# Kernel tuning notes

Hardware: AMD Instinct MI355X
Metric: run time of the kernel (lower is better)

The kernel has to match this reference:

```python
import jax, jax.numpy as jnp
import numpy as np

N_NODES = 100000
N_EDGES = 1600000
EMB = 128
N_LAYER = 5
X_DIM = 178
E_DIM = 18
BN_EPS = 1e-5


def setup_inputs() -> dict:
    key = jax.random.key(0)
    ks = jax.random.split(key, 20)
    s = 0.05  # weight scale
    inp = {}
    inp["x"] = jax.random.normal(ks[0], (N_NODES, X_DIM), jnp.float32)
    inp["edge_attr"] = jax.random.uniform(ks[1], (N_EDGES, E_DIM), jnp.float32)
    # input MLP (178 -> emb -> emb, LeakyReLU 0.1)
    inp["iw1"] = jax.random.normal(ks[2], (X_DIM, EMB), jnp.float32) * s
    inp["ib1"] = jax.random.normal(ks[3], (EMB,), jnp.float32) * s
    inp["iw2"] = jax.random.normal(ks[4], (EMB, EMB), jnp.float32) * s
    inp["ib2"] = jax.random.normal(ks[5], (EMB,), jnp.float32) * s
    # per-layer edge embedding MLP (18 -> emb -> emb, LeakyReLU 0.1)
    inp["ew1"] = jax.random.normal(ks[6], (N_LAYER, E_DIM, EMB), jnp.float32) * s
    inp["eb1"] = jax.random.normal(ks[7], (N_LAYER, EMB), jnp.float32) * s
    inp["ew2"] = jax.random.normal(ks[8], (N_LAYER, EMB, EMB), jnp.float32) * s
    inp["eb2"] = jax.random.normal(ks[9], (N_LAYER, EMB), jnp.float32) * s
    # per-layer GIN update MLP (emb -> 2emb -> emb, ReLU)
    inp["mw1"] = jax.random.normal(ks[10], (N_LAYER, EMB, 2 * EMB), jnp.float32) * s
    inp["mb1"] = jax.random.normal(ks[11], (N_LAYER, 2 * EMB), jnp.float32) * s
    inp["mw2"] = jax.random.normal(ks[12], (N_LAYER, 2 * EMB, EMB), jnp.float32) * s
    inp["mb2"] = jax.random.normal(ks[13], (N_LAYER, EMB), jnp.float32) * s
    # per-layer BatchNorm affine params
    inp["gamma"] = jnp.ones((N_LAYER, EMB), jnp.float32)
    inp["beta"] = jnp.zeros((N_LAYER, EMB), jnp.float32)
    inp["edge_index"] = jax.random.randint(ks[14], (2, N_EDGES), 0, N_NODES)
    return inp


def _leaky(v):
    return jnp.where(v > 0, v, 0.1 * v)


def reference(x, edge_attr, iw1, ib1, iw2, ib2, ew1, eb1, ew2, eb2,
              mw1, mb1, mw2, mb2, gamma, beta, edge_index):
    src = edge_index[0]  # x_j gathered from source nodes (PyG source_to_target)
    dst = edge_index[1]
    n = x.shape[0]

    # input node MLP with LeakyReLU(0.1)
    h = _leaky(x @ iw1 + ib1) @ iw2 + ib2  # [N, EMB]

    for l in range(N_LAYER):
        # edge embeddings for real edges: [E, EMB]
        ee = _leaky(edge_attr @ ew1[l] + eb1[l]) @ ew2[l] + eb2[l]
        # self-loop edges have zero edge_attr -> constant embedding vector [EMB]
        self_e = _leaky(eb1[l]) @ ew2[l] + eb2[l]
        # message = x_j + edge_emb; aggregate (add) at destination, plus self-loop term
        msg = h[src] + ee
        aggr = jax.ops.segment_sum(msg, dst, num_segments=n) + h + self_e
        # GIN update MLP (ReLU)
        hh = jnp.maximum(aggr @ mw1[l] + mb1[l], 0.0) @ mw2[l] + mb2[l]
        # BatchNorm1d (training mode: batch stats, biased variance)
        mean = hh.mean(axis=0)
        var = hh.var(axis=0)
        hh = (hh - mean) / jnp.sqrt(var + BN_EPS) * gamma[l] + beta[l]
        if l < N_LAYER - 1:
            hh = jnp.maximum(hh, 0.0)  # ReLU on all but last layer; dropout p=0 is a no-op
        h = hh

    return h  # JK == 'last'
```

## Files before the change

kernel.cpp:

```cpp
#include <hip/hip_runtime.h>
#include <hip/hip_bf16.h>
#include <hip/hip_fp16.h>
#include <cstdint>
#include <cstddef>

#define NNODES 100000
#define NEDGES 1600000
#define EMBD 128
#define NLAYER 5
#define XDIM 178
#define EDIM 18
#define BNEPS 1e-5f

typedef __attribute__((ext_vector_type(8))) short short8;
typedef __attribute__((ext_vector_type(8))) unsigned short ushort8;
typedef __attribute__((ext_vector_type(4))) float f32x4;

static __device__ __forceinline__ float leakyf(float v){ return v > 0.f ? v : 0.1f*v; }
static __device__ __forceinline__ unsigned short f2b(float v){
  __hip_bfloat16 b = __float2bfloat16(v);
  return *reinterpret_cast<unsigned short*>(&b);
}
static __device__ __forceinline__ float b2f(unsigned short u){
  __hip_bfloat16 b = *reinterpret_cast<__hip_bfloat16*>(&u);
  return __bfloat162float(b);
}
static __device__ __forceinline__ unsigned short f2h(float v){
  __half h = __float2half(v);
  return *reinterpret_cast<unsigned short*>(&h);
}
static __device__ __forceinline__ float h2f(unsigned short u){
  __half h = *reinterpret_cast<__half*>(&u);
  return __half2float(h);
}

__global__ __launch_bounds__(256) void k_hist(const int* __restrict__ dst, int* __restrict__ cnt){
  int e = blockIdx.x*256 + threadIdx.x;
  if (e < NEDGES) atomicAdd(&cnt[dst[e]], 1);
}

__global__ __launch_bounds__(256) void k_scan1(const int* __restrict__ cnt, int* __restrict__ rowptr,
                                               int* __restrict__ bsum){
  __shared__ int s[256];
  int t = threadIdx.x, i = blockIdx.x*256 + t;
  int v = (i < NNODES) ? cnt[i] : 0;
  s[t] = v; __syncthreads();
  for (int off=1; off<256; off<<=1){
    int x = (t>=off) ? s[t-off] : 0; __syncthreads();
    s[t] += x; __syncthreads();
  }
  if (i < NNODES) rowptr[i+1] = s[t];
  if (t == 255) bsum[blockIdx.x] = s[t];
}

__global__ __launch_bounds__(512) void k_scan2(const int* __restrict__ bsum, int* __restrict__ boff, int nb){
  __shared__ int s[512];
  int t = threadIdx.x;
  int v = (t < nb) ? bsum[t] : 0;
  s[t] = v; __syncthreads();
  for (int off=1; off<512; off<<=1){
    int x = (t>=off) ? s[t-off] : 0; __syncthreads();
    s[t] += x; __syncthreads();
  }
  if (t < nb) boff[t] = s[t] - v;
}

__global__ __launch_bounds__(256) void k_scan3(int* __restrict__ rowptr, const int* __restrict__ boff){
  int i = blockIdx.x*256 + threadIdx.x;
  if (i < NNODES) rowptr[i+1] += boff[i>>8];
  if (i == 0) rowptr[0] = 0;
}

__global__ __launch_bounds__(256) void k_curcopy(const int* __restrict__ rowptr, int* __restrict__ cursor){
  int i = blockIdx.x*256 + threadIdx.x;
  if (i < NNODES) cursor[i] = rowptr[i];
}

__global__ __launch_bounds__(256) void k_fill_new(const int* __restrict__ src, const int* __restrict__ dst,
                                                  const float* __restrict__ ea, int* __restrict__ cursor,
                                                  int* __restrict__ srcp, unsigned short* __restrict__ eap24){
  int e = blockIdx.x*256 + threadIdx.x;
  if (e >= NEDGES) return;
  int pos = atomicAdd(&cursor[dst[e]], 1);
  srcp[pos] = src[e];
  const float* a = ea + (size_t)e*EDIM;
  ushort8 r0, r1, r2;
  #pragma unroll
  for (int k=0;k<8;++k)  r0[k] = f2b(a[k]);
  #pragma unroll
  for (int k=0;k<8;++k)  r1[k] = f2b(a[8+k]);
  #pragma unroll
  for (int k=0;k<8;++k)  r2[k] = 0;
  r2[0] = f2b(a[16]); r2[1] = f2b(a[17]);
  r2[2] = 0x3F80;
  unsigned short* o = eap24 + (size_t)pos*24;
  *reinterpret_cast<ushort8*>(o)      = r0;
  *reinterpret_cast<ushort8*>(o + 8)  = r1;
  *reinterpret_cast<ushort8*>(o + 16) = r2;
}

__global__ __launch_bounds__(256) void k_fill(const int* __restrict__ src, const int* __restrict__ dst,
                                              const float* __restrict__ ea, int* __restrict__ cursor,
                                              int* __restrict__ perm, int* __restrict__ srcp,
                                              float* __restrict__ eap){
  int e = blockIdx.x*256 + threadIdx.x;
  if (e >= NEDGES) return;
  int pos = atomicAdd(&cursor[dst[e]], 1);
  perm[pos] = e;
  srcp[pos] = src[e];
  if (eap){
    const float* a = ea + (size_t)e*EDIM;
    float* o = eap + (size_t)pos*EDIM;
    #pragma unroll
    for (int k=0;k<EDIM;++k) o[k] = a[k];
  }
}

__global__ __launch_bounds__(128) void k_selfe(const float* __restrict__ eb1, const float* __restrict__ ew2,
                                               const float* __restrict__ eb2, float* __restrict__ selfe){
  int l = blockIdx.x, c = threadIdx.x;
  const float* b1 = eb1 + l*EMBD;
  const float* w2 = ew2 + (size_t)l*EMBD*EMBD;
  float acc = eb2[l*EMBD + c];
  for (int j=0;j<EMBD;++j) acc += leakyf(b1[j]) * w2[j*EMBD + c];
  selfe[l*EMBD + c] = acc;
}

__global__ __launch_bounds__(256) void k_wc(const float* __restrict__ ew2, const float* __restrict__ mw1,
                                            float* __restrict__ wc){
  int idx = blockIdx.x*256 + threadIdx.x;
  int l = idx >> 15, rem = idx & 32767;
  int i = rem >> 8, n = rem & 255;
  const float* e = ew2 + (size_t)l*EMBD*EMBD + i*EMBD;
  const float* m = mw1 + (size_t)l*EMBD*2*EMBD + n;
  float acc = 0.f;
  #pragma unroll 4
  for (int j=0;j<EMBD;++j) acc += e[j]*m[(size_t)j*2*EMBD];
  wc[idx] = acc;
}

__global__ __launch_bounds__(256) void k_pack(const float* __restrict__ s1, int rows1,
                                              const float* __restrict__ s2, int Kreal,
                                              int Kpad, int N, __hip_bfloat16* __restrict__ out){
  int idx = blockIdx.x*256 + threadIdx.x;
  if (idx >= Kpad*N) return;
  int k = idx / N, n = idx - k*N;
  float v = 0.f;
  if (k < rows1) v = s1[(size_t)k*N + n];
  else if (k < Kreal) v = s2[(size_t)(k-rows1)*N + n];
  unsigned short hi = f2b(v);
  unsigned short lo = f2b(v - b2f(hi));
  size_t o = (size_t)(k>>5)*N*32 + (size_t)n*32 + (k&31);
  unsigned short* po = (unsigned short*)out;
  po[o] = hi;
  po[(size_t)Kpad*N + o] = lo;
}

__global__ __launch_bounds__(256) void k_gather_h(
    const float* __restrict__ h, const unsigned short* __restrict__ hh,
    const int* __restrict__ rowptr, const int* __restrict__ srcp,
    const float* __restrict__ eb2l, const float* __restrict__ selfel,
    float* __restrict__ base)
{
  int tid = threadIdx.x;
  int li = tid & 31;
  int c4 = li*4;
  float4 sf4 = *(const float4*)(selfel + c4);
  float4 e24 = *(const float4*)(eb2l + c4);
  int slot = blockIdx.x*8 + (tid>>5);
  const int NS = gridDim.x*8;
  for (int node = slot; node < NNODES; node += NS){
    int rs = rowptr[node], re = rowptr[node+1];
    f32x4 b = (f32x4)0.f;
    for (int c0 = rs; c0 < re; c0 += 8){
      int cnt = re - c0;
      #pragma unroll
      for (int p=0;p<8;++p){
        int e = c0 + p; if (e > re-1) e = re-1;
        float m = (p < cnt) ? 1.f : 0.f;
        int sp = srcp[e];
        uint2 hv = *(const uint2*)(hh + (size_t)sp*EMBD + c4);
        b[0] = fmaf(m, h2f((unsigned short)(hv.x & 0xffffu)), b[0]);
        b[1] = fmaf(m, h2f((unsigned short)(hv.x >> 16)),     b[1]);
        b[2] = fmaf(m, h2f((unsigned short)(hv.y & 0xffffu)), b[2]);
        b[3] = fmaf(m, h2f((unsigned short)(hv.y >> 16)),     b[3]);
      }
    }
    float deg = (float)(re - rs);
    float4 hn = *(const float4*)(h + (size_t)node*EMBD + c4);
    float4 o;
    o.x = b[0] + hn.x + sf4.x + deg*e24.x;
    o.y = b[1] + hn.y + sf4.y + deg*e24.y;
    o.z = b[2] + hn.z + sf4.z + deg*e24.z;
    o.w = b[3] + hn.w + sf4.w + deg*e24.w;
    *(float4*)(base + (size_t)node*EMBD + c4) = o;
  }
}

__global__ __launch_bounds__(256) void k_gather(
    const float* __restrict__ h, const int* __restrict__ rowptr,
    const int* __restrict__ srcp,
    const float* __restrict__ eb2l, const float* __restrict__ selfel,
    float* __restrict__ base)
{
  int tid = threadIdx.x;
  int li = tid & 31;
  int c4 = li*4;
  float4 sf4 = *(const float4*)(selfel + c4);
  float4 e24 = *(const float4*)(eb2l + c4);
  int slot = blockIdx.x*8 + (tid>>5);
  const int NS = gridDim.x*8;
  for (int node = slot; node < NNODES; node += NS){
    int rs = rowptr[node], re = rowptr[node+1];
    f32x4 b = (f32x4)0.f;
    for (int c0 = rs; c0 < re; c0 += 8){
      int cnt = re - c0;
      #pragma unroll
      for (int p=0;p<8;++p){
        int e = c0 + p; if (e > re-1) e = re-1;
        float m = (p < cnt) ? 1.f : 0.f;
        int sp = srcp[e];
        float4 hv = *(const float4*)(h + (size_t)sp*EMBD + c4);
        b[0] = fmaf(m, hv.x, b[0]);
        b[1] = fmaf(m, hv.y, b[1]);
        b[2] = fmaf(m, hv.z, b[2]);
        b[3] = fmaf(m, hv.w, b[3]);
      }
    }
    float deg = (float)(re - rs);
    float4 hn = *(const float4*)(h + (size_t)node*EMBD + c4);
    float4 o;
    o.x = b[0] + hn.x + sf4.x + deg*e24.x;
    o.y = b[1] + hn.y + sf4.y + deg*e24.y;
    o.z = b[2] + hn.z + sf4.z + deg*e24.z;
    o.w = b[3] + hn.w + sf4.w + deg*e24.w;
    *(float4*)(base + (size_t)node*EMBD + c4) = o;
  }
}

__global__ __launch_bounds__(256, 4) void k_s1(
    const int* __restrict__ rowptr, const unsigned short* __restrict__ eap24,
    const float* __restrict__ ew1l, const float* __restrict__ eb1l,
    float* __restrict__ S1)
{
  int tid = threadIdx.x;
  int lane = tid & 63;
  int lr = lane & 15, kb = lane >> 4;

  short8 bh[8], bl[8];
  #pragma unroll
  for (int nf=0; nf<8; ++nf){
    int col = nf*16 + lr;
    ushort8 hh8, ll8;
    #pragma unroll
    for (int j=0;j<8;++j){
      int k = kb*8 + j;
      float v = 0.f;
      if (k < EDIM) v = ew1l[k*EMBD + col];
      else if (k == EDIM) v = eb1l[col];
      unsigned short hi = f2b(v);
      hh8[j] = hi;
      ll8[j] = f2b(v - b2f(hi));
    }
    bh[nf] = *reinterpret_cast<short8*>(&hh8);
    bl[nf] = *reinterpret_cast<short8*>(&ll8);
  }

  auto loadC = [&](int c0, int re)->short8{
    int cnt = re - c0;
    int idx = c0 + lr; if (idx > re-1) idx = re-1;
    short8 af = (short8)0;
    if (kb < 3){
      ushort8 t = *reinterpret_cast<const ushort8*>(eap24 + (size_t)idx*24 + kb*8);
      af = *reinterpret_cast<short8*>(&t);
    }
    if (lr >= cnt) af = (short8)0;
    return af;
  };

  int wid = blockIdx.x*4 + (tid>>6);
  const int NW = gridDim.x*4;
  for (int nA = wid; nA < NNODES; nA += 2*NW){
    int nB = nA + NW;
    bool hasB = (nB < NNODES);
    int rsA = rowptr[nA], reA = rowptr[nA+1];
    int rsB = 0, reB = 0;
    if (hasB){ rsB = rowptr[nB]; reB = rowptr[nB+1]; }
    float sA[8], sB[8];
    #pragma unroll
    for (int nf=0;nf<8;++nf){ sA[nf]=0.f; sB[nf]=0.f; }
    int cA = rsA, cB = rsB;
    while (cA < reA || cB < reB){
      bool dA = cA < reA, dB = cB < reB;
      short8 afA = (short8)0, afB = (short8)0;
      if (dA) afA = loadC(cA, reA);
      if (dB) afB = loadC(cB, reB);
      if (dA){
        #pragma unroll
        for (int nf=0;nf<8;++nf){
          f32x4 acc = (f32x4)0.f;
          acc = __builtin_amdgcn_mfma_f32_16x16x32_bf16(afA, bl[nf], acc, 0,0,0);
          acc = __builtin_amdgcn_mfma_f32_16x16x32_bf16(afA, bh[nf], acc, 0,0,0);
          #pragma unroll
          for (int j=0;j<4;++j){
            float v = acc[j];
            sA[nf] = fmaf(0.55f, v, sA[nf]);
            sA[nf] = fmaf(0.45f, fabsf(v), sA[nf]);
          }
        }
      }
      if (dB){
        #pragma unroll
        for (int nf=0;nf<8;++nf){
          f32x4 acc = (f32x4)0.f;
          acc = __builtin_amdgcn_mfma_f32_16x16x32_bf16(afB, bl[nf], acc, 0,0,0);
          acc = __builtin_amdgcn_mfma_f32_16x16x32_bf16(afB, bh[nf], acc, 0,0,0);
          #pragma unroll
          for (int j=0;j<4;++j){
            float v = acc[j];
            sB[nf] = fmaf(0.55f, v, sB[nf]);
            sB[nf] = fmaf(0.45f, fabsf(v), sB[nf]);
          }
        }
      }
      cA += 16; cB += 16;
    }

    {
      #pragma unroll
      for (int nf=0;nf<8;++nf){
        float v = sA[nf];
        v += __shfl_xor(v, 16);
        v += __shfl_xor(v, 32);
        sA[nf] = v;
      }
      float va = sA[0], vb = sA[1];
      if (kb == 1){ va = sA[2]; vb = sA[3]; }
      if (kb == 2){ va = sA[4]; vb = sA[5]; }
      if (kb == 3){ va = sA[6]; vb = sA[7]; }
      S1[(size_t)nA*EMBD + kb*32 + lr]      = va;
      S1[(size_t)nA*EMBD + kb*32 + 16 + lr] = vb;
    }
    if (hasB){
      #pragma unroll
      for (int nf=0;nf<8;++nf){
        float v = sB[nf];
        v += __shfl_xor(v, 16);
        v += __shfl_xor(v, 32);
        sB[nf] = v;
      }
      float va = sB[0], vb = sB[1];
      if (kb == 1){ va = sB[2]; vb = sB[3]; }
      if (kb == 2){ va = sB[4]; vb = sB[5]; }
      if (kb == 3){ va = sB[6]; vb = sB[7]; }
      S1[(size_t)nB*EMBD + kb*32 + lr]      = va;
      S1[(size_t)nB*EMBD + kb*32 + 16 + lr] = vb;
    }
  }
}

__global__ __launch_bounds__(256) void k_edge(
    const float* __restrict__ h, const int* __restrict__ rowptr,
    const int* __restrict__ perm, const int* __restrict__ srcp,
    const float* __restrict__ edge_attr, const float* __restrict__ eaperm,
    const float* __restrict__ ew1l, const float* __restrict__ eb1l,
    const float* __restrict__ eb2l, const float* __restrict__ selfel,
    float* __restrict__ S1, float* __restrict__ base)
{
  __shared__ float w1s[EDIM*EMBD];
  __shared__ float b1s[EMBD];
  int tid = threadIdx.x;
  for (int i = tid; i < EDIM*EMBD; i += 256) w1s[i] = ew1l[i];
  if (tid < EMBD) b1s[tid] = eb1l[tid];
  __syncthreads();
  int lane = tid & 63;
  int node = blockIdx.x*4 + (tid >> 6);
  if (node >= NNODES) return;
  int rs = rowptr[node], re = rowptr[node+1];
  int c0 = lane*2;
  float s1x=0.f, s1y=0.f, bx=0.f, by=0.f;
  for (int i = rs; i < re; ++i){
    int s = __builtin_amdgcn_readfirstlane(srcp[i]);
    const float* ea;
    if (eaperm){
      ea = eaperm + (size_t)__builtin_amdgcn_readfirstlane(i)*EDIM;
    } else {
      ea = edge_attr + (size_t)__builtin_amdgcn_readfirstlane(perm[i])*EDIM;
    }
    float2 hs = *(const float2*)(h + (size_t)s*EMBD + c0);
    bx += hs.x; by += hs.y;
    float d0 = b1s[c0], d1 = b1s[c0+1];
    #pragma unroll
    for (int k=0;k<EDIM;++k){
      float av = ea[k];
      d0 += av * w1s[k*EMBD + c0];
      d1 += av * w1s[k*EMBD + c0 + 1];
    }
    s1x += leakyf(d0); s1y += leakyf(d1);
  }
  float deg = (float)(re - rs);
  float2 hv = *(const float2*)(h + (size_t)node*EMBD + c0);
  *(float2*)(S1 + (size_t)node*EMBD + c0) = make_float2(s1x, s1y);
  float bvx = bx + hv.x + selfel[c0]   + deg*eb2l[c0];
  float bvy = by + hv.y + selfel[c0+1] + deg*eb2l[c0+1];
  *(float2*)(base + (size_t)node*EMBD + c0) = make_float2(bvx, bvy);
}

template<int BN, int WGM, int WGN, bool ALO, int ACT, bool STATS, bool OBF16, bool CONCAT, bool KCHK, bool ABF16>
__global__ __launch_bounds__(512) void k_mgemm(
    const float* __restrict__ Af, const float* __restrict__ A1,
    const __hip_bfloat16* __restrict__ Ab,
    int M, int Kreal, int Kpad, int lda,
    const __hip_bfloat16* __restrict__ Bp,
    const float* __restrict__ bias,
    float* __restrict__ Cf, __hip_bfloat16* __restrict__ Cb, int ldc,
    float* __restrict__ stats, unsigned short* __restrict__ Ch)
{
  static_assert(WGM*WGN == 8, "8 waves");
  constexpr int BM = 128;
  constexpr int MF = BM/(16*WGM);
  constexpr int NF = BN/(16*WGN);
  constexpr int LDS_ROW = 40;
  __shared__ __align__(16) unsigned short Ah[BM*LDS_ROW];
  __shared__ __align__(16) unsigned short Al[ALO ? BM*LDS_ROW : 8];
  __shared__ float ssum[STATS ? BN : 4];
  __shared__ float ssq [STATS ? BN : 4];

  int tid = threadIdx.x;
  int row0 = blockIdx.x*BM;
  int w = tid >> 6, lane = tid & 63;
  int wm = w / WGN, wn = w % WGN;
  int lr = lane & 15, kb = lane >> 4;
  int wrow = wm*MF*16, wcol = wn*NF*16;

  if (STATS && tid < BN){ ssum[tid] = 0.f; ssq[tid] = 0.f; }

  f32x4 acc[MF][NF];
  #pragma unroll
  for (int a=0;a<MF;++a)
    #pragma unroll
    for (int b=0;b<NF;++b) acc[a][b] = (f32x4)0.f;

  const size_t planeSz = (size_t)Kpad*BN;
  int sr = tid >> 2;
  int skq = (tid & 3)*8;
  int grow = row0 + sr;
  const int KS = Kpad >> 5;

  for (int ks = 0; ks < KS; ++ks){
    int k0 = ks << 5;
    int kg = k0 + skq;
    ushort8 hv, lv;
    if (ABF16){
      short8 raw = (short8)0;
      if (grow < M) raw = *reinterpret_cast<const short8*>((const unsigned short*)Ab + (size_t)grow*lda + kg);
      hv = *reinterpret_cast<ushort8*>(&raw);
    } else {
      float v[8];
      if (KCHK){
        #pragma unroll
        for (int i=0;i<8;++i)
          v[i] = (grow < M && kg+i < Kreal) ? Af[(size_t)grow*lda + kg + i] : 0.f;
      } else {
        const float* s;
        if (CONCAT) s = (kg < EMBD) ? (Af + (size_t)grow*lda + kg) : (A1 + (size_t)grow*lda + (kg - EMBD));
        else        s = Af + (size_t)grow*lda + kg;
        float4 p0 = make_float4(0,0,0,0), p1 = make_float4(0,0,0,0);
        if (grow < M){ p0 = *(const float4*)s; p1 = *(const float4*)(s+4); }
        v[0]=p0.x; v[1]=p0.y; v[2]=p0.z; v[3]=p0.w;
        v[4]=p1.x; v[5]=p1.y; v[6]=p1.z; v[7]=p1.w;
      }
      #pragma unroll
      for (int i=0;i<8;++i){
        unsigned short h16 = f2b(v[i]);
        hv[i] = h16;
        if (ALO) lv[i] = f2b(v[i] - b2f(h16));
      }
    }
    __syncthreads();
    *reinterpret_cast<ushort8*>(&Ah[sr*LDS_ROW + skq]) = hv;
    if (ALO && !ABF16) *reinterpret_cast<ushort8*>(&Al[sr*LDS_ROW + skq]) = lv;
    __syncthreads();

    short8 ah[MF], al[MF];
    #pragma unroll
    for (int mf=0; mf<MF; ++mf){
      int r = (wrow + mf*16 + lr)*LDS_ROW + kb*8;
      ah[mf] = *reinterpret_cast<const short8*>(&Ah[r]);
      if (ALO) al[mf] = *reinterpret_cast<const short8*>(&Al[r]);
    }
    const unsigned short* bb = (const unsigned short*)Bp + (size_t)ks*BN*32;
    short8 bh[NF], blv[NF];
    #pragma unroll
    for (int nf=0; nf<NF; ++nf){
      size_t off = (size_t)(wcol + nf*16 + lr)*32 + kb*8;
      bh[nf] = *reinterpret_cast<const short8*>(bb + off);
      blv[nf] = *reinterpret_cast<const short8*>(bb + planeSz + off);
    }
    #pragma unroll
    for (int mf=0; mf<MF; ++mf){
      #pragma unroll
      for (int nf=0; nf<NF; ++nf){
        acc[mf][nf] = __builtin_amdgcn_mfma_f32_16x16x32_bf16(ah[mf], bh[nf], acc[mf][nf], 0, 0, 0);
        acc[mf][nf] = __builtin_amdgcn_mfma_f32_16x16x32_bf16(ah[mf], blv[nf], acc[mf][nf], 0, 0, 0);
        if (ALO)
          acc[mf][nf] = __builtin_amdgcn_mfma_f32_16x16x32_bf16(al[mf], bh[nf], acc[mf][nf], 0, 0, 0);
      }
    }
  }

  float bcol[NF];
  #pragma unroll
  for (int nf=0; nf<NF; ++nf) bcol[nf] = bias ? bias[wcol + nf*16 + lr] : 0.f;
  float s[NF], sq[NF];
  #pragma unroll
  for (int nf=0; nf<NF; ++nf){ s[nf]=0.f; sq[nf]=0.f; }

  #pragma unroll
  for (int mf=0; mf<MF; ++mf){
    #pragma unroll
    for (int j=0; j<4; ++j){
      int r = row0 + wrow + mf*16 + kb*4 + j;
      if (r < M){
        #pragma unroll
        for (int nf=0; nf<NF; ++nf){
          int c = wcol + nf*16 + lr;
          float v = acc[mf][nf][j] + bcol[nf];
          if (ACT == 1) v = leakyf(v);
          if (ACT == 2) v = fmaxf(v, 0.f);
          if (OBF16) Cb[(size_t)r*ldc + c] = __float2bfloat16(v);
          else       Cf[(size_t)r*ldc + c] = v;
          if (Ch) Ch[(size_t)r*ldc + c] = f2h(v);
          if (STATS){ s[nf] += v; sq[nf] += v*v; }
        }
      }
    }
  }
  if (STATS){
    #pragma unroll
    for (int nf=0; nf<NF; ++nf){
      atomicAdd(&ssum[wcol + nf*16 + lr], s[nf]);
      atomicAdd(&ssq [wcol + nf*16 + lr], sq[nf]);
    }
    __syncthreads();
    if (tid < BN){
      atomicAdd(&stats[tid], ssum[tid]);
      atomicAdd(&stats[BN + tid], ssq[tid]);
    }
  }
}

__global__ __launch_bounds__(256) void k_bn(const float* __restrict__ hh, const float* __restrict__ stats,
                                            const float* __restrict__ gamma, const float* __restrict__ beta,
                                            float* __restrict__ out, unsigned short* __restrict__ outh,
                                            int dorelu){
  int idx = blockIdx.x*256 + threadIdx.x;
  if (idx >= NNODES*(EMBD/4)) return;
  int c0 = (idx & (EMBD/4 - 1)) * 4;
  float4 v = *(const float4*)(hh + (size_t)idx*4);
  float o[4] = {v.x, v.y, v.z, v.w};
  const float invN = 1.f / (float)NNODES;
  #pragma unroll
  for (int i=0;i<4;++i){
    int c = c0 + i;
    float mean = stats[c] * invN;
    float var  = stats[EMBD + c] * invN - mean*mean;
    float inv  = rsqrtf(fmaxf(var, 0.f) + BNEPS);
    float y = (o[i] - mean) * inv * gamma[c] + beta[c];
    if (dorelu) y = fmaxf(y, 0.f);
    o[i] = y;
  }
  *(float4*)(out + (size_t)idx*4) = make_float4(o[0],o[1],o[2],o[3]);
  if (outh){
    ushort8 dummy;
    unsigned short p0 = f2h(o[0]), p1 = f2h(o[1]), p2 = f2h(o[2]), p3 = f2h(o[3]);
    uint2 pk;
    pk.x = (unsigned)p0 | ((unsigned)p1 << 16);
    pk.y = (unsigned)p2 | ((unsigned)p3 << 16);
    *reinterpret_cast<uint2*>(outh + (size_t)idx*4) = pk;
    (void)dummy;
  }
}

extern "C" void kernel_launch(void* const* d_in, const int* in_sizes, int n_in,
                              void* d_out, int out_size, void* d_ws, size_t ws_size,
                              hipStream_t stream)
{
  const float* x   = (const float*)d_in[0];
  const float* ea  = (const float*)d_in[1];
  const float* iw1 = (const float*)d_in[2];
  const float* ib1 = (const float*)d_in[3];
  const float* iw2 = (const float*)d_in[4];
  const float* ib2 = (const float*)d_in[5];
  const float* ew1 = (const float*)d_in[6];
  const float* eb1 = (const float*)d_in[7];
  const float* ew2 = (const float*)d_in[8];
  const float* eb2 = (const float*)d_in[9];
  const float* mw1 = (const float*)d_in[10];
  const float* mb1 = (const float*)d_in[11];
  const float* mw2 = (const float*)d_in[12];
  const float* mb2 = (const float*)d_in[13];
  const float* gamma = (const float*)d_in[14];
  const float* beta  = (const float*)d_in[15];
  const int* eidx = (const int*)d_in[16];
  const int* srcI = eidx;
  const int* dstI = eidx + NEDGES;

  char* p = (char*)d_ws;
  auto alloc = [&](size_t bytes)->char*{
    char* r = p; p += (bytes + 255) & ~(size_t)255; return r;
  };
  float* hbuf  = (float*)alloc((size_t)NNODES*EMBD*4);
  float* S1    = (float*)alloc((size_t)NNODES*EMBD*4);
  float* base  = (float*)alloc((size_t)NNODES*EMBD*4);
  __hip_bfloat16* tbuf = (__hip_bfloat16*)alloc((size_t)NNODES*2*EMBD*2);
  int* perm   = (int*)alloc((size_t)NEDGES*4);
  int* srcp   = (int*)alloc((size_t)NEDGES*4);
  int* rowptr = (int*)alloc((size_t)(NNODES+1)*4);
  int* cursor = (int*)alloc((size_t)NNODES*4);
  int* bsum   = (int*)alloc(4096);
  int* boff   = (int*)alloc(4096);
  float* selfe = (float*)alloc(NLAYER*EMBD*4);
  float* stats = (float*)alloc(2*EMBD*4);
  float* wc    = (float*)alloc((size_t)NLAYER*EMBD*2*EMBD*4);
  __hip_bfloat16* Bi1 = (__hip_bfloat16*)alloc((size_t)192*EMBD*2*2);
  __hip_bfloat16* Bi2 = (__hip_bfloat16*)alloc((size_t)EMBD*EMBD*2*2);
  __hip_bfloat16* B1  = (__hip_bfloat16*)alloc((size_t)NLAYER*256*256*2*2);
  __hip_bfloat16* B2  = (__hip_bfloat16*)alloc((size_t)NLAYER*256*EMBD*2*2);
  size_t used = (size_t)(p - (char*)d_ws);

  bool use_new = (ws_size >= used + (size_t)NEDGES*24*2 + 256);
  unsigned short* eap24 = nullptr;
  float* eaperm = nullptr;
  if (use_new) eap24 = (unsigned short*)alloc((size_t)NEDGES*24*2);
  else if (ws_size >= used + (size_t)NEDGES*EDIM*4 + 256)
    eaperm = (float*)alloc((size_t)NEDGES*EDIM*4);

  used = (size_t)(p - (char*)d_ws);
  bool use_h16 = use_new && (ws_size >= used + (size_t)NNODES*EMBD*2 + 256);
  unsigned short* hh16 = nullptr;
  if (use_h16) hh16 = (unsigned short*)alloc((size_t)NNODES*EMBD*2);

  hipMemsetAsync(cursor, 0, (size_t)NNODES*4, stream);
  k_hist<<<(NEDGES+255)/256, 256, 0, stream>>>(dstI, cursor);
  int nb = (NNODES+255)/256;
  k_scan1<<<nb, 256, 0, stream>>>(cursor, rowptr, bsum);
  k_scan2<<<1, 512, 0, stream>>>(bsum, boff, nb);
  k_scan3<<<(NNODES+255)/256, 256, 0, stream>>>(rowptr, boff);
  k_curcopy<<<(NNODES+255)/256, 256, 0, stream>>>(rowptr, cursor);
  if (use_new)
    k_fill_new<<<(NEDGES+255)/256, 256, 0, stream>>>(srcI, dstI, ea, cursor, srcp, eap24);
  else
    k_fill<<<(NEDGES+255)/256, 256, 0, stream>>>(srcI, dstI, ea, cursor, perm, srcp, eaperm);
  k_selfe<<<NLAYER, EMBD, 0, stream>>>(eb1, ew2, eb2, selfe);

  k_wc<<<(NLAYER*EMBD*2*EMBD)/256, 256, 0, stream>>>(ew2, mw1, wc);
  k_pack<<<(192*EMBD+255)/256, 256, 0, stream>>>(iw1, XDIM, iw1, XDIM, 192, EMBD, Bi1);
  k_pack<<<(EMBD*EMBD+255)/256, 256, 0, stream>>>(iw2, EMBD, iw2, EMBD, EMBD, EMBD, Bi2);
  for (int l=0; l<NLAYER; ++l){
    k_pack<<<(256*256+255)/256, 256, 0, stream>>>(
        wc + (size_t)l*EMBD*2*EMBD, EMBD, mw1 + (size_t)l*EMBD*2*EMBD, 256, 256, 256,
        B1 + (size_t)l*256*256*2);
    k_pack<<<(256*EMBD+255)/256, 256, 0, stream>>>(
        mw2 + (size_t)l*2*EMBD*EMBD, 256, mw2, 256, 256, EMBD,
        B2 + (size_t)l*256*EMBD*2);
  }

  const int gx = (NNODES + 127)/128;

  k_mgemm<128,4,2, true,1,false,false,false,true ,false><<<gx, 512, 0, stream>>>(
      x, nullptr, nullptr, NNODES, XDIM, 192, XDIM, Bi1, ib1, S1, nullptr, EMBD, nullptr, nullptr);
  k_mgemm<128,4,2, true,0,false,false,false,false,false><<<gx, 512, 0, stream>>>(
      S1, nullptr, nullptr, NNODES, EMBD, EMBD, EMBD, Bi2, ib2, hbuf, nullptr, EMBD, nullptr,
      use_h16 ? hh16 : nullptr);

  for (int l=0; l<NLAYER; ++l){
    hipMemsetAsync(stats, 0, 2*EMBD*4, stream);
    if (use_new){
      if (use_h16)
        k_gather_h<<<2048, 256, 0, stream>>>(
            hbuf, hh16, rowptr, srcp, eb2 + l*EMBD, selfe + l*EMBD, base);
      else
        k_gather<<<2048, 256, 0, stream>>>(
            hbuf, rowptr, srcp, eb2 + l*EMBD, selfe + l*EMBD, base);
      k_s1<<<1024, 256, 0, stream>>>(
          rowptr, eap24, ew1 + (size_t)l*EDIM*EMBD, eb1 + l*EMBD, S1);
    } else {
      k_edge<<<NNODES/4, 256, 0, stream>>>(
          hbuf, rowptr, perm, srcp, ea, eaperm,
          ew1 + (size_t)l*EDIM*EMBD, eb1 + l*EMBD, eb2 + l*EMBD, selfe + l*EMBD,
          S1, base);
    }
    k_mgemm<256,2,4, true,2,false,true ,true ,false,false><<<gx, 512, 0, stream>>>(
        S1, base, nullptr, NNODES, 256, 256, EMBD, B1 + (size_t)l*256*256*2,
        mb1 + l*2*EMBD, nullptr, tbuf, 2*EMBD, nullptr, nullptr);
    k_mgemm<128,4,2, false,0,true ,false,false,false,true ><<<gx, 512, 0, stream>>>(
        nullptr, nullptr, tbuf, NNODES, 256, 256, 2*EMBD, B2 + (size_t)l*256*EMBD*2,
        mb2 + l*EMBD, S1, nullptr, EMBD, stats, nullptr);
    float* outp = (l == NLAYER-1) ? (float*)d_out : hbuf;
    unsigned short* outh = (l < NLAYER-1 && use_h16) ? hh16 : nullptr;
    k_bn<<<(NNODES*(EMBD/4)+255)/256, 256, 0, stream>>>(
        S1, stats, gamma + l*EMBD, beta + l*EMBD, outp, outh, (l < NLAYER-1) ? 1 : 0);
  }
}
```

Before: 2.021 ms.

## Fuse gather and edge-MLP kernels into one launch with block specialization

After: 1.997 ms. About the same (-1.2%).

```diff
diff --git a/kernel.cpp b/kernel.cpp
--- a/kernel.cpp
+++ b/kernel.cpp
@@ -76,22 +76,36 @@
   if (i < NNODES) cursor[i] = rowptr[i];
 }
 
-__global__ __launch_bounds__(256) void k_fill_new(const int* __restrict__ src, const int* __restrict__ dst,
-                                                  const float* __restrict__ ea, int* __restrict__ cursor,
-                                                  int* __restrict__ srcp, unsigned short* __restrict__ eap24){
+__global__ __launch_bounds__(256) void k_fill_pos(const int* __restrict__ dst, int* __restrict__ cursor,
+                                                  int* __restrict__ einv){
   int e = blockIdx.x*256 + threadIdx.x;
   if (e >= NEDGES) return;
   int pos = atomicAdd(&cursor[dst[e]], 1);
+  einv[pos] = e;
+}
+
+__global__ __launch_bounds__(256) void k_fill_ea(const int* __restrict__ einv, const int* __restrict__ src,
+                                                 const float* __restrict__ ea,
+                                                 int* __restrict__ srcp, unsigned short* __restrict__ eap24){
+  int pos = blockIdx.x*256 + threadIdx.x;
+  if (pos >= NEDGES) return;
+  int e = einv[pos];
   srcp[pos] = src[e];
   const float* a = ea + (size_t)e*EDIM;
+  float v[18];
+  #pragma unroll
+  for (int k=0;k<9;++k){
+    float2 t = *(const float2*)(a + 2*k);
+    v[2*k] = t.x; v[2*k+1] = t.y;
+  }
   ushort8 r0, r1, r2;
   #pragma unroll
-  for (int k=0;k<8;++k)  r0[k] = f2b(a[k]);
-  #pragma unroll
-  for (int k=0;k<8;++k)  r1[k] = f2b(a[8+k]);
-  #pragma unroll
-  for (int k=0;k<8;++k)  r2[k] = 0;
-  r2[0] = f2b(a[16]); r2[1] = f2b(a[17]);
+  for (int k=0;k<8;++k) r0[k] = f2b(v[k]);
+  #pragma unroll
+  for (int k=0;k<8;++k) r1[k] = f2b(v[8+k]);
+  #pragma unroll
+  for (int k=0;k<8;++k) r2[k] = 0;
+  r2[0] = f2b(v[16]); r2[1] = f2b(v[17]);
   r2[2] = 0x3F80;
   unsigned short* o = eap24 + (size_t)pos*24;
   *reinterpret_cast<ushort8*>(o)      = r0;
@@ -156,205 +170,161 @@
   po[(size_t)Kpad*N + o] = lo;
 }
 
-__global__ __launch_bounds__(256) void k_gather_h(
-    const float* __restrict__ h, const unsigned short* __restrict__ hh,
-    const int* __restrict__ rowptr, const int* __restrict__ srcp,
+__global__ __launch_bounds__(256) void k_edge2(
+    const unsigned short* __restrict__ hh, const int* __restrict__ rowptr,
+    const int* __restrict__ srcp, const unsigned short* __restrict__ eap24,
+    const float* __restrict__ ew1l, const float* __restrict__ eb1l,
     const float* __restrict__ eb2l, const float* __restrict__ selfel,
-    float* __restrict__ base)
+    float* __restrict__ S1, float* __restrict__ base, int GG)
 {
   int tid = threadIdx.x;
-  int li = tid & 31;
-  int c4 = li*4;
-  float4 sf4 = *(const float4*)(selfel + c4);
-  float4 e24 = *(const float4*)(eb2l + c4);
-  int slot = blockIdx.x*8 + (tid>>5);
-  const int NS = gridDim.x*8;
-  for (int node = slot; node < NNODES; node += NS){
-    int rs = rowptr[node], re = rowptr[node+1];
-    f32x4 b = (f32x4)0.f;
-    for (int c0 = rs; c0 < re; c0 += 8){
+  if ((int)blockIdx.x < GG){
+    int li = tid & 31;
+    int c4 = li*4;
+    float4 sf4 = *(const float4*)(selfel + c4);
+    float4 e24 = *(const float4*)(eb2l + c4);
+    int slot = blockIdx.x*8 + (tid>>5);
+    const int NS = GG*8;
+    for (int node = slot; node < NNODES; node += NS){
+      int rs = rowptr[node], re = rowptr[node+1];
+      f32x4 b = (f32x4)0.f;
+      for (int c0 = rs; c0 < re; c0 += 8){
+        int cnt = re - c0;
+        #pragma unroll
+        for (int p=0;p<8;++p){
+          int e = c0 + p; if (e > re-1) e = re-1;
+          float m = (p < cnt) ? 1.f : 0.f;
+          int sp = srcp[e];
+          uint2 hv = *(const uint2*)(hh + (size_t)sp*EMBD + c4);
+          b[0] = fmaf(m, h2f((unsigned short)(hv.x & 0xffffu)), b[0]);
+          b[1] = fmaf(m, h2f((unsigned short)(hv.x >> 16)),     b[1]);
+          b[2] = fmaf(m, h2f((unsigned short)(hv.y & 0xffffu)), b[2]);
+          b[3] = fmaf(m, h2f((unsigned short)(hv.y >> 16)),     b[3]);
+        }
+      }
+      float deg = (float)(re - rs);
+      uint2 hn = *(const uint2*)(hh + (size_t)node*EMBD + c4);
+      float4 o;
+      o.x = b[0] + h2f((unsigned short)(hn.x & 0xffffu)) + sf4.x + deg*e24.x;
+      o.y = b[1] + h2f((unsigned short)(hn.x >> 16))     + sf4.y + deg*e24.y;
+      o.z = b[2] + h2f((unsigned short)(hn.y & 0xffffu)) + sf4.z + deg*e24.z;
+      o.w = b[3] + h2f((unsigned short)(hn.y >> 16))     + sf4.w + deg*e24.w;
+      *(float4*)(base + (size_t)node*EMBD + c4) = o;
+    }
+  } else {
+    int lane = tid & 63;
+    int lr = lane & 15, kb = lane >> 4;
+
+    short8 bh[8], bl[8];
+    #pragma unroll
+    for (int nf=0; nf<8; ++nf){
+      int col = nf*16 + lr;
+      ushort8 hh8, ll8;
+      #pragma unroll
+      for (int j=0;j<8;++j){
+        int k = kb*8 + j;
+        float v = 0.f;
+        if (k < EDIM) v = ew1l[k*EMBD + col];
+        else if (k == EDIM) v = eb1l[col];
+        unsigned short hi = f2b(v);
+        hh8[j] = hi;
+        ll8[j] = f2b(v - b2f(hi));
+      }
+      bh[nf] = *reinterpret_cast<short8*>(&hh8);
+      bl[nf] = *reinterpret_cast<short8*>(&ll8);
+    }
+
+    auto loadC = [&](int c0, int re)->short8{
       int cnt = re - c0;
+      int idx = c0 + lr; if (idx > re-1) idx = re-1;
+      short8 af = (short8)0;
+      if (kb < 3){
+        ushort8 t = *reinterpret_cast<const ushort8*>(eap24 + (size_t)idx*24 + kb*8);
+        af = *reinterpret_cast<short8*>(&t);
+      }
+      if (lr >= cnt) af = (short8)0;
+      return af;
+    };
+
+    const int GS = gridDim.x - GG;
+    int wid = (blockIdx.x - GG)*4 + (tid>>6);
+    const int NW = GS*4;
+    for (int nA = wid; nA < NNODES; nA += 2*NW){
+      int nB = nA + NW;
+      bool hasB = (nB < NNODES);
+      int rsA = rowptr[nA], reA = rowptr[nA+1];
+      int rsB = 0, reB = 0;
+      if (hasB){ rsB = rowptr[nB]; reB = rowptr[nB+1]; }
+      float sA[8], sB[8];
       #pragma unroll
-      for (int p=0;p<8;++p){
-        int e = c0 + p; if (e > re-1) e = re-1;
-        float m = (p < cnt) ? 1.f : 0.f;
-        int sp = srcp[e];
-        uint2 hv = *(const uint2*)(hh + (size_t)sp*EMBD + c4);
-        b[0] = fmaf(m, h2f((unsigned short)(hv.x & 0xffffu)), b[0]);
-        b[1] = fmaf(m, h2f((unsigned short)(hv.x >> 16)),     b[1]);
-        b[2] = fmaf(m, h2f((unsigned short)(hv.y & 0xffffu)), b[2]);
-        b[3] = fmaf(m, h2f((unsigned short)(hv.y >> 16)),     b[3]);
-      }
-    }
-    float deg = (float)(re - rs);
-    float4 hn = *(const float4*)(h + (size_t)node*EMBD + c4);
-    float4 o;
-    o.x = b[0] + hn.x + sf4.x + deg*e24.x;
-    o.y = b[1] + hn.y + sf4.y + deg*e24.y;
-    o.z = b[2] + hn.z + sf4.z + deg*e24.z;
-    o.w = b[3] + hn.w + sf4.w + deg*e24.w;
-    *(float4*)(base + (size_t)node*EMBD + c4) = o;
-  }
-}
-
-__global__ __launch_bounds__(256) void k_gather(
-    const float* __restrict__ h, const int* __restrict__ rowptr,
-    const int* __restrict__ srcp,
-    const float* __restrict__ eb2l, const float* __restrict__ selfel,
-    float* __restrict__ base)
-{
-  int tid = threadIdx.x;
-  int li = tid & 31;
-  int c4 = li*4;
-  float4 sf4 = *(const float4*)(selfel + c4);
-  float4 e24 = *(const float4*)(eb2l + c4);
-  int slot = blockIdx.x*8 + (tid>>5);
-  const int NS = gridDim.x*8;
-  for (int node = slot; node < NNODES; node += NS){
-    int rs = rowptr[node], re = rowptr[node+1];
-    f32x4 b = (f32x4)0.f;
-    for (int c0 = rs; c0 < re; c0 += 8){
-      int cnt = re - c0;
-      #pragma unroll
-      for (int p=0;p<8;++p){
-        int e = c0 + p; if (e > re-1) e = re-1;
-        float m = (p < cnt) ? 1.f : 0.f;
-        int sp = srcp[e];
-        float4 hv = *(const float4*)(h + (size_t)sp*EMBD + c4);
-        b[0] = fmaf(m, hv.x, b[0]);
-        b[1] = fmaf(m, hv.y, b[1]);
-        b[2] = fmaf(m, hv.z, b[2]);
-        b[3] = fmaf(m, hv.w, b[3]);
-      }
-    }
-    float deg = (float)(re - rs);
-    float4 hn = *(const float4*)(h + (size_t)node*EMBD + c4);
-    float4 o;
-    o.x = b[0] + hn.x + sf4.x + deg*e24.x;
-    o.y = b[1] + hn.y + sf4.y + deg*e24.y;
-    o.z = b[2] + hn.z + sf4.z + deg*e24.z;
-    o.w = b[3] + hn.w + sf4.w + deg*e24.w;
-    *(float4*)(base + (size_t)node*EMBD + c4) = o;
-  }
-}
-
-__global__ __launch_bounds__(256, 4) void k_s1(
-    const int* __restrict__ rowptr, const unsigned short* __restrict__ eap24,
-    const float* __restrict__ ew1l, const float* __restrict__ eb1l,
-    float* __restrict__ S1)
-{
-  int tid = threadIdx.x;
-  int lane = tid & 63;
-  int lr = lane & 15, kb = lane >> 4;
-
-  short8 bh[8], bl[8];
-  #pragma unroll
-  for (int nf=0; nf<8; ++nf){
-    int col = nf*16 + lr;
-    ushort8 hh8, ll8;
-    #pragma unroll
-    for (int j=0;j<8;++j){
-      int k = kb*8 + j;
-      float v = 0.f;
-      if (k < EDIM) v = ew1l[k*EMBD + col];
-      else if (k == EDIM) v = eb1l[col];
-      unsigned short hi = f2b(v);
-      hh8[j] = hi;
-      ll8[j] = f2b(v - b2f(hi));
-    }
-    bh[nf] = *reinterpret_cast<short8*>(&hh8);
-    bl[nf] = *reinterpret_cast<short8*>(&ll8);
-  }
-
-  auto loadC = [&](int c0, int re)->short8{
-    int cnt = re - c0;
-    int idx = c0 + lr; if (idx > re-1) idx = re-1;
-    short8 af = (short8)0;
-    if (kb < 3){
-      ushort8 t = *reinterpret_cast<const ushort8*>(eap24 + (size_t)idx*24 + kb*8);
-      af = *reinterpret_cast<short8*>(&t);
-    }
-    if (lr >= cnt) af = (short8)0;
-    return af;
-  };
-
-  int wid = blockIdx.x*4 + (tid>>6);
-  const int NW = gridDim.x*4;
-  for (int nA = wid; nA < NNODES; nA += 2*NW){
-    int nB = nA + NW;
-    bool hasB = (nB < NNODES);
-    int rsA = rowptr[nA], reA = rowptr[nA+1];
-    int rsB = 0, reB = 0;
-    if (hasB){ rsB = rowptr[nB]; reB = rowptr[nB+1]; }
-    float sA[8], sB[8];
-    #pragma unroll
-    for (int nf=0;nf<8;++nf){ sA[nf]=0.f; sB[nf]=0.f; }
-    int cA = rsA, cB = rsB;
-    while (cA < reA || cB < reB){
-      bool dA = cA < reA, dB = cB < reB;
-      short8 afA = (short8)0, afB = (short8)0;
-      if (dA) afA = loadC(cA, reA);
-      if (dB) afB = loadC(cB, reB);
-      if (dA){
+      for (int nf=0;nf<8;++nf){ sA[nf]=0.f; sB[nf]=0.f; }
+      int cA = rsA, cB = rsB;
+      while (cA < reA || cB < reB){
+        bool dA = cA < reA, dB = cB < reB;
+        short8 afA = (short8)0, afB = (short8)0;
+        if (dA) afA = loadC(cA, reA);
+        if (dB) afB = loadC(cB, reB);
+        if (dA){
+          #pragma unroll
+          for (int nf=0;nf<8;++nf){
+            f32x4 acc = (f32x4)0.f;
+            acc = __builtin_amdgcn_mfma_f32_16x16x32_bf16(afA, bl[nf], acc, 0,0,0);
+            acc = __builtin_amdgcn_mfma_f32_16x16x32_bf16(afA, bh[nf], acc, 0,0,0);
+            #pragma unroll
+            for (int j=0;j<4;++j){
+              float v = acc[j];
+              sA[nf] = fmaf(0.55f, v, sA[nf]);
+              sA[nf] = fmaf(0.45f, fabsf(v), sA[nf]);
+            }
+          }
+        }
+        if (dB){
+          #pragma unroll
+          for (int nf=0;nf<8;++nf){
+            f32x4 acc = (f32x4)0.f;
+            acc = __builtin_amdgcn_mfma_f32_16x16x32_bf16(afB, bl[nf], acc, 0,0,0);
+            acc = __builtin_amdgcn_mfma_f32_16x16x32_bf16(afB, bh[nf], acc, 0,0,0);
+            #pragma unroll
+            for (int j=0;j<4;++j){
+              float v = acc[j];
+              sB[nf] = fmaf(0.55f, v, sB[nf]);
+              sB[nf] = fmaf(0.45f, fabsf(v), sB[nf]);
+            }
+          }
+        }
+        cA += 16; cB += 16;
+      }
+
+      {
         #pragma unroll
         for (int nf=0;nf<8;++nf){
-          f32x4 acc = (f32x4)0.f;
-          acc = __builtin_amdgcn_mfma_f32_16x16x32_bf16(afA, bl[nf], acc, 0,0,0);
-          acc = __builtin_amdgcn_mfma_f32_16x16x32_bf16(afA, bh[nf], acc, 0,0,0);
-          #pragma unroll
-          for (int j=0;j<4;++j){
-            float v = acc[j];
-            sA[nf] = fmaf(0.55f, v, sA[nf]);
-            sA[nf] = fmaf(0.45f, fabsf(v), sA[nf]);
-          }
+          float v = sA[nf];
+          v += __shfl_xor(v, 16);
+          v += __shfl_xor(v, 32);
+          sA[nf] = v;
         }
-      }
-      if (dB){
+        float va = sA[0], vb = sA[1];
+        if (kb == 1){ va = sA[2]; vb = sA[3]; }
+        if (kb == 2){ va = sA[4]; vb = sA[5]; }
+        if (kb == 3){ va = sA[6]; vb = sA[7]; }
+        S1[(size_t)nA*EMBD + kb*32 + lr]      = va;
+        S1[(size_t)nA*EMBD + kb*32 + 16 + lr] = vb;
+      }
+      if (hasB){
         #pragma unroll
         for (int nf=0;nf<8;++nf){
-          f32x4 acc = (f32x4)0.f;
-          acc = __builtin_amdgcn_mfma_f32_16x16x32_bf16(afB, bl[nf], acc, 0,0,0);
-          acc = __builtin_amdgcn_mfma_f32_16x16x32_bf16(afB, bh[nf], acc, 0,0,0);
-          #pragma unroll
-          for (int j=0;j<4;++j){
-            float v = acc[j];
-            sB[nf] = fmaf(0.55f, v, sB[nf]);
-            sB[nf] = fmaf(0.45f, fabsf(v), sB[nf]);
-          }
+          float v = sB[nf];
+          v += __shfl_xor(v, 16);
+          v += __shfl_xor(v, 32);
+          sB[nf] = v;
         }
-      }
-      cA += 16; cB += 16;
-    }
-
-    {
-      #pragma unroll
-      for (int nf=0;nf<8;++nf){
-        float v = sA[nf];
-        v += __shfl_xor(v, 16);
-        v += __shfl_xor(v, 32);
-        sA[nf] = v;
-      }
-      float va = sA[0], vb = sA[1];
-      if (kb == 1){ va = sA[2]; vb = sA[3]; }
-      if (kb == 2){ va = sA[4]; vb = sA[5]; }
-      if (kb == 3){ va = sA[6]; vb = sA[7]; }
-      S1[(size_t)nA*EMBD + kb*32 + lr]      = va;
-      S1[(size_t)nA*EMBD + kb*32 + 16 + lr] = vb;
-    }
-    if (hasB){
-      #pragma unroll
-      for (int nf=0;nf<8;++nf){
-        float v = sB[nf];
-        v += __shfl_xor(v, 16);
-        v += __shfl_xor(v, 32);
-        sB[nf] = v;
-      }
-      float va = sB[0], vb = sB[1];
-      if (kb == 1){ va = sB[2]; vb = sB[3]; }
-      if (kb == 2){ va = sB[4]; vb = sB[5]; }
-      if (kb == 3){ va = sB[6]; vb = sB[7]; }
-      S1[(size_t)nB*EMBD + kb*32 + lr]      = va;
-      S1[(size_t)nB*EMBD + kb*32 + 16 + lr] = vb;
+        float va = sB[0], vb = sB[1];
+        if (kb == 1){ va = sB[2]; vb = sB[3]; }
+        if (kb == 2){ va = sB[4]; vb = sB[5]; }
+        if (kb == 3){ va = sB[6]; vb = sB[7]; }
+        S1[(size_t)nB*EMBD + kb*32 + lr]      = va;
+        S1[(size_t)nB*EMBD + kb*32 + 16 + lr] = vb;
+      }
     }
   }
 }
@@ -570,15 +540,12 @@
     if (dorelu) y = fmaxf(y, 0.f);
     o[i] = y;
   }
-  *(float4*)(out + (size_t)idx*4) = make_float4(o[0],o[1],o[2],o[3]);
+  if (out) *(float4*)(out + (size_t)idx*4) = make_float4(o[0],o[1],o[2],o[3]);
   if (outh){
-    ushort8 dummy;
-    unsigned short p0 = f2h(o[0]), p1 = f2h(o[1]), p2 = f2h(o[2]), p3 = f2h(o[3]);
     uint2 pk;
-    pk.x = (unsigned)p0 | ((unsigned)p1 << 16);
-    pk.y = (unsigned)p2 | ((unsigned)p3 << 16);
+    pk.x = (unsigned)f2h(o[0]) | ((unsigned)f2h(o[1]) << 16);
+    pk.y = (unsigned)f2h(o[2]) | ((unsigned)f2h(o[3]) << 16);
     *reinterpret_cast<uint2*>(outh + (size_t)idx*4) = pk;
-    (void)dummy;
   }
 }
 
@@ -629,17 +596,16 @@
   __hip_bfloat16* B2  = (__hip_bfloat16*)alloc((size_t)NLAYER*256*EMBD*2*2);
   size_t used = (size_t)(p - (char*)d_ws);
 
-  bool use_new = (ws_size >= used + (size_t)NEDGES*24*2 + 256);
+  bool use_new = (ws_size >= used + (size_t)NEDGES*24*2 + (size_t)NNODES*EMBD*2 + 512);
   unsigned short* eap24 = nullptr;
+  unsigned short* hh16 = nullptr;
   float* eaperm = nullptr;
-  if (use_new) eap24 = (unsigned short*)alloc((size_t)NEDGES*24*2);
-  else if (ws_size >= used + (size_t)NEDGES*EDIM*4 + 256)
+  if (use_new){
+    eap24 = (unsigned short*)alloc((size_t)NEDGES*24*2);
+    hh16  = (unsigned short*)alloc((size_t)NNODES*EMBD*2);
+  } else if (ws_size >= used + (size_t)NEDGES*EDIM*4 + 256){
     eaperm = (float*)alloc((size_t)NEDGES*EDIM*4);
-
-  used = (size_t)(p - (char*)d_ws);
-  bool use_h16 = use_new && (ws_size >= used + (size_t)NNODES*EMBD*2 + 256);
-  unsigned short* hh16 = nullptr;
-  if (use_h16) hh16 = (unsigned short*)alloc((size_t)NNODES*EMBD*2);
+  }
 
   hipMemsetAsync(cursor, 0, (size_t)NNODES*4, stream);
   k_hist<<<(NEDGES+255)/256, 256, 0, stream>>>(dstI, cursor);
@@ -648,10 +614,12 @@
   k_scan2<<<1, 512, 0, stream>>>(bsum, boff, nb);
   k_scan3<<<(NNODES+255)/256, 256, 0, stream>>>(rowptr, boff);
   k_curcopy<<<(NNODES+255)/256, 256, 0, stream>>>(rowptr, cursor);
-  if (use_new)
-    k_fill_new<<<(NEDGES+255)/256, 256, 0, stream>>>(srcI, dstI, ea, cursor, srcp, eap24);
-  else
+  if (use_new){
+    k_fill_pos<<<(NEDGES+255)/256, 256, 0, stream>>>(dstI, cursor, perm);
+    k_fill_ea<<<(NEDGES+255)/256, 256, 0, stream>>>(perm, srcI, ea, srcp, eap24);
+  } else {
     k_fill<<<(NEDGES+255)/256, 256, 0, stream>>>(srcI, dstI, ea, cursor, perm, srcp, eaperm);
+  }
   k_selfe<<<NLAYER, EMBD, 0, stream>>>(eb1, ew2, eb2, selfe);
 
   k_wc<<<(NLAYER*EMBD*2*EMBD)/256, 256, 0, stream>>>(ew2, mw1, wc);
@@ -672,19 +640,15 @@
       x, nullptr, nullptr, NNODES, XDIM, 192, XDIM, Bi1, ib1, S1, nullptr, EMBD, nullptr, nullptr);
   k_mgemm<128,4,2, true,0,false,false,false,false,false><<<gx, 512, 0, stream>>>(
       S1, nullptr, nullptr, NNODES, EMBD, EMBD, EMBD, Bi2, ib2, hbuf, nullptr, EMBD, nullptr,
-      use_h16 ? hh16 : nullptr);
+      use_new ? hh16 : nullptr);
 
   for (int l=0; l<NLAYER; ++l){
     hipMemsetAsync(stats, 0, 2*EMBD*4, stream);
     if (use_new){
-      if (use_h16)
-        k_gather_h<<<2048, 256, 0, stream>>>(
-            hbuf, hh16, rowptr, srcp, eb2 + l*EMBD, selfe + l*EMBD, base);
-      else
-        k_gather<<<2048, 256, 0, stream>>>(
-            hbuf, rowptr, srcp, eb2 + l*EMBD, selfe + l*EMBD, base);
-      k_s1<<<1024, 256, 0, stream>>>(
-          rowptr, eap24, ew1 + (size_t)l*EDIM*EMBD, eb1 + l*EMBD, S1);
+      k_edge2<<<2048, 256, 0, stream>>>(
+          hh16, rowptr, srcp, eap24,
+          ew1 + (size_t)l*EDIM*EMBD, eb1 + l*EMBD, eb2 + l*EMBD, selfe + l*EMBD,
+          S1, base, 1280);
     } else {
       k_edge<<<NNODES/4, 256, 0, stream>>>(
           hbuf, rowptr, perm, srcp, ea, eaperm,
@@ -697,8 +661,10 @@
     k_mgemm<128,4,2, false,0,true ,false,false,false,true ><<<gx, 512, 0, stream>>>(
         nullptr, nullptr, tbuf, NNODES, 256, 256, 2*EMBD, B2 + (size_t)l*256*EMBD*2,
         mb2 + l*EMBD, S1, nullptr, EMBD, stats, nullptr);
-    float* outp = (l == NLAYER-1) ? (float*)d_out : hbuf;
-    unsigned short* outh = (l < NLAYER-1 && use_h16) ? hh16 : nullptr;
+    float* outp; unsigned short* outh;
+    if (l == NLAYER-1){ outp = (float*)d_out; outh = nullptr; }
+    else if (use_new) { outp = nullptr;       outh = hh16;    }
+    else              { outp = hbuf;          outh = nullptr; }
     k_bn<<<(NNODES*(EMBD/4)+255)/256, 256, 0, stream>>>(
         S1, stats, gamma + l*EMBD, beta + l*EMBD, outp, outh, (l < NLAYER-1) ? 1 : 0);
   }
```
